# Optimization experiments

Measured on AMD Instinct MI355X. Metric: run time of the kernel, lower is better.

Reference implementation:

```python
import jax, jax.numpy as jnp
import numpy as np

H, D, K = 8, 64, 9           # new num heads, head size, conv kernel size
A = H * D                    # all_head_size = 512
HID = 2 * A                  # input hidden size = 1024
STD = 0.02


def setup_inputs() -> dict:
    key = jax.random.key(0)
    ks = jax.random.split(key, 16)
    B, S = 4, 2048
    f = jnp.float32
    inp = {
        'hidden_states': jax.random.normal(ks[0], (B, S, HID), f),
        'Wq': jax.random.normal(ks[1], (A, A), f) * STD,
        'bq': jnp.zeros((A,), f),
        'Wk': jax.random.normal(ks[2], (A, A), f) * STD,
        'bk': jnp.zeros((A,), f),
        'Wv': jax.random.normal(ks[3], (A, A), f) * STD,
        'bv': jnp.zeros((A,), f),
        'dw_w': jax.random.normal(ks[4], (A, 1, K), f) * STD,   # depthwise conv (groups=A)
        'pw_w': jax.random.normal(ks[5], (A, A, 1), f) * STD,   # pointwise 1x1 conv
        'sep_b': jnp.zeros((A, 1), f),                          # SeparableConv1D bias
        'Wck': jax.random.normal(ks[6], (H * K, A), f) * STD,   # conv_kernel_layer
        'bck': jnp.zeros((H * K,), f),
        'Wco': jax.random.normal(ks[7], (A, A), f) * STD,       # conv_out_layer
        'bco': jnp.zeros((A,), f),
    }
    return inp


def reference(hidden_states, Wq, bq, Wk, bk, Wv, bv, dw_w, pw_w, sep_b, Wck, bck, Wco, bco):
    B, S, _ = hidden_states.shape
    hs_attn = hidden_states[:, :, :A]
    hs_conv = hidden_states[:, :, A:]

    q = hs_attn @ Wq.T + bq
    k = hs_attn @ Wk.T + bk
    v = hs_attn @ Wv.T + bv

    # SeparableConv1D on (B, A, S): depthwise then pointwise, plus bias
    x = hs_conv.transpose(0, 2, 1)
    x = jax.lax.conv_general_dilated(
        x, dw_w, window_strides=(1,), padding=[(K // 2, K // 2)],
        feature_group_count=A, dimension_numbers=('NCH', 'OIH', 'NCH'))
    x = jnp.einsum('bcs,oc->bos', x, pw_w[:, :, 0]) + sep_b
    mixed_key_conv = x.transpose(0, 2, 1)            # (B,S,A)

    # per-token softmax conv kernel
    conv_attn = mixed_key_conv * hs_conv
    ckl = (conv_attn @ Wck.T + bck).reshape(B, S, H, K)
    ckl = jax.nn.softmax(ckl, axis=-1)               # softmax over kernel taps

    # dynamic-span lightweight convolution (unfold -> batched matmul)
    col = hs_conv @ Wco.T + bco                      # (B,S,A)
    pad = jnp.pad(col, ((0, 0), (K // 2, K // 2), (0, 0)))
    windows = jnp.stack([pad[:, i:i + S] for i in range(K)], axis=-1)  # (B,S,A,K)
    windows = windows.reshape(B, S, H, D, K)
    conv_out = jnp.einsum('bshdk,bshk->bshd', windows, ckl)            # (B,S,H,D)

    # standard self-attention
    qh = q.reshape(B, S, H, D).transpose(0, 2, 1, 3)
    kh = k.reshape(B, S, H, D).transpose(0, 2, 1, 3)
    vh = v.reshape(B, S, H, D).transpose(0, 2, 1, 3)
    scale = jnp.asarray(1.0 / np.sqrt(D), q.dtype)
    scores = jnp.einsum('bhqd,bhkd->bhqk', qh, kh) * scale
    probs = jax.nn.softmax(scores, axis=-1)
    ctx = jnp.einsum('bhqk,bhkd->bqhd', probs, vh)   # (B,S,H,D)

    out = jnp.concatenate([ctx, conv_out], axis=2)   # (B,S,2H,D)
    return out.reshape(B, S, HID)
```

## Files before the change

kernel.cpp:

```cpp
#include <hip/hip_runtime.h>
#include <hip/hip_bf16.h>

#define NH   8
#define HD   64
#define KW   9
#define AD   512
#define HIDD 1024
#define BB   4
#define SS   2048
#define MTOK (BB*SS)
#define WSZ  262144

typedef __attribute__((ext_vector_type(8))) short short8;
typedef __attribute__((ext_vector_type(4))) float floatx4;
typedef __attribute__((ext_vector_type(16))) float floatx16;

__device__ __forceinline__ short f2bf(float f) {
    unsigned u = __float_as_uint(f);
    u = (u + 0x7FFFu + ((u >> 16) & 1u)) >> 16;
    return (short)u;
}
__device__ __forceinline__ float bf2f(short s) {
    return __uint_as_float(((unsigned)(unsigned short)s) << 16);
}
__device__ __forceinline__ float exp2_raw(float x) {
    return __builtin_amdgcn_exp2f(x);
}
__device__ __forceinline__ unsigned pkbf2(float a, float b) {
    unsigned d;
    asm("v_cvt_pk_bf16_f32 %0, %1, %2" : "=v"(d) : "v"(a), "v"(b));
    return d;
}
__device__ __forceinline__ void gl2lds16(const short* g, short* l) {
    __builtin_amdgcn_global_load_lds(
        (const __attribute__((address_space(1))) void*)g,
        (__attribute__((address_space(3))) void*)l, 16, 0, 0);
}

__global__ __launch_bounds__(256) void prep_kernel(
    const float* __restrict__ hs,
    const float* __restrict__ pw, const float* __restrict__ Wco,
    const float* __restrict__ Wq, const float* __restrict__ Wk,
    const float* __restrict__ Wv, const float* __restrict__ Wck,
    const float* __restrict__ dw,
    short* __restrict__ hsb, short* __restrict__ wb, short* __restrict__ x1)
{
    __shared__ float wl[KW * AD];
    const int bid = blockIdx.x, tid = threadIdx.x;

    if (bid < 4096) {
        int idx = bid * 256 + tid;
        const float* s = hs + (long)idx * 8;
        float4 a = *(const float4*)s, c = *(const float4*)(s + 4);
        short8 o;
        o[0]=f2bf(a.x); o[1]=f2bf(a.y); o[2]=f2bf(a.z); o[3]=f2bf(a.w);
        o[4]=f2bf(c.x); o[5]=f2bf(c.y); o[6]=f2bf(c.z); o[7]=f2bf(c.w);
        *(short8*)(hsb + (long)idx * 8) = o;
    } else if (bid < 4768) {
        int idx = (bid - 4096) * 256 + tid;
        int e0 = idx * 8;
        short8 o;
        if (e0 < 5 * WSZ) {
            int w = e0 >> 18, off = e0 & (WSZ - 1);
            const float* src = (w == 0) ? pw : (w == 1) ? Wco : (w == 2) ? Wq
                             : (w == 3) ? Wk : Wv;
            float4 a = *(const float4*)(src + off), c = *(const float4*)(src + off + 4);
            o[0]=f2bf(a.x); o[1]=f2bf(a.y); o[2]=f2bf(a.z); o[3]=f2bf(a.w);
            o[4]=f2bf(c.x); o[5]=f2bf(c.y); o[6]=f2bf(c.z); o[7]=f2bf(c.w);
        } else {
            int off = e0 - 5 * WSZ;
            int row = off >> 9, col = off & 511;
            if (row < NH * KW) {
                const float* src = Wck + row * AD + col;
                float4 a = *(const float4*)src, c = *(const float4*)(src + 4);
                o[0]=f2bf(a.x); o[1]=f2bf(a.y); o[2]=f2bf(a.z); o[3]=f2bf(a.w);
                o[4]=f2bf(c.x); o[5]=f2bf(c.y); o[6]=f2bf(c.z); o[7]=f2bf(c.w);
            } else {
                for (int i = 0; i < 8; ++i) o[i] = 0;
            }
        }
        *(short8*)(wb + e0) = o;
    } else {
        for (int t = tid; t < KW * AD; t += 256) {
            int c = t / KW, k = t - c * KW;
            wl[k * AD + c] = dw[t];
        }
        __syncthreads();
        int idx = (bid - 4768) * 256 + tid;
        int c8  = (idx & 63) * 8;
        int tok = idx >> 6;
        int s   = tok & (SS - 1);
        int b   = tok >> 11;
        const float* base = hs + (long)(b * SS) * HIDD + AD + c8;
        float acc[8];
#pragma unroll
        for (int i = 0; i < 8; ++i) acc[i] = 0.f;
#pragma unroll
        for (int kk = 0; kk < KW; ++kk) {
            int ss2 = s + kk - KW / 2;
            if (ss2 >= 0 && ss2 < SS) {
                const float* hp = base + (long)ss2 * HIDD;
                float4 h0 = *(const float4*)hp;
                float4 h1 = *(const float4*)(hp + 4);
                float4 w0 = *(const float4*)(wl + kk * AD + c8);
                float4 w1 = *(const float4*)(wl + kk * AD + c8 + 4);
                acc[0] += w0.x * h0.x; acc[1] += w0.y * h0.y;
                acc[2] += w0.z * h0.z; acc[3] += w0.w * h0.w;
                acc[4] += w1.x * h1.x; acc[5] += w1.y * h1.y;
                acc[6] += w1.z * h1.z; acc[7] += w1.w * h1.w;
            }
        }
        short8 o;
#pragma unroll
        for (int i = 0; i < 8; ++i) o[i] = f2bf(acc[i]);
        *(short8*)(x1 + (long)tok * AD + c8) = o;
    }
}

template<int FM, int FN, int MODE>
__device__ __forceinline__ void gemm_body(
    int bx, int by, short* Sm,
    const short* __restrict__ X, int ldx, int xoff,
    const short* __restrict__ W,
    const float* __restrict__ b0p, const float* __restrict__ b1p,
    const float* __restrict__ b2p,
    const short* __restrict__ mulp, int mul_ld, int mul_off,
    void* __restrict__ Cout, short* __restrict__ vtout,
    int ldc, int N, int Kd, float oscale)
{
    constexpr int TM = 32 * FM, TN = 32 * FN;
    constexpr int SLOT = (TM + TN) * 64;
    const int tid  = threadIdx.x;
    const int wv   = tid >> 6, lane = tid & 63;
    const int ln   = lane & 15, quad = lane >> 4;
    const int wm   = wv >> 1, wn = wv & 1;
    const int m0 = bx * TM, n0 = by * TN;

    floatx4 acc[FM][FN];
#pragma unroll
    for (int i = 0; i < FM; ++i)
#pragma unroll
        for (int j = 0; j < FN; ++j) acc[i][j] = (floatx4){0.f, 0.f, 0.f, 0.f};

    const short* xbase = X + (long)m0 * ldx + xoff;
    const short* wbase = W + (long)n0 * Kd;

    auto stage = [&](int k0, int slot) {
        short* As = Sm + slot * SLOT;
        short* Bs = As + TM * 64;
#pragma unroll
        for (int g = tid; g < TM * 8; g += 256) {
            int m = g >> 3, p = g & 7, gk = p ^ (m & 7);
            gl2lds16(xbase + (long)m * ldx + k0 + gk * 8, &As[g * 8]);
        }
#pragma unroll
        for (int g = tid; g < TN * 8; g += 256) {
            int m = g >> 3, p = g & 7, gk = p ^ (m & 7);
            gl2lds16(wbase + (long)m * Kd + k0 + gk * 8, &Bs[g * 8]);
        }
    };
    auto compute = [&](int slot) {
        const short* As = Sm + slot * SLOT;
        const short* Bs = As + TM * 64;
#pragma unroll
        for (int half = 0; half < 2; ++half) {
            short8 afr[FM], bfr[FN];
#pragma unroll
            for (int i = 0; i < FM; ++i) {
                int p = (half * 4 + quad) ^ (ln & 7);
                afr[i] = *(const short8*)&As[(wm * 16 * FM + i * 16 + ln) * 64 + p * 8];
            }
#pragma unroll
            for (int j = 0; j < FN; ++j) {
                int p = (half * 4 + quad) ^ (ln & 7);
                bfr[j] = *(const short8*)&Bs[(wn * 16 * FN + j * 16 + ln) * 64 + p * 8];
            }
#pragma unroll
            for (int i = 0; i < FM; ++i)
#pragma unroll
                for (int j = 0; j < FN; ++j)
                    acc[i][j] = __builtin_amdgcn_mfma_f32_16x16x32_bf16(
                        afr[i], bfr[j], acc[i][j], 0, 0, 0);
        }
    };

    stage(0, 0);
    asm volatile("s_waitcnt vmcnt(0)" ::: "memory");
    __builtin_amdgcn_s_barrier();
    asm volatile("" ::: "memory");

    const int nk = Kd >> 6;
    int slot = 0;
    for (int t = 0; t < nk - 1; ++t) {
        stage((t + 1) * 64, slot ^ 1);
        compute(slot);
        asm volatile("s_waitcnt vmcnt(0)" ::: "memory");
        __builtin_amdgcn_s_barrier();
        asm volatile("" ::: "memory");
        slot ^= 1;
    }
    compute(slot);

    if constexpr (MODE == 3) {
        if (n0 >= 1024) {
            __syncthreads();
            short* T = Sm;
#pragma unroll
            for (int j = 0; j < FN; ++j) {
                int nl = wn * 16 * FN + j * 16 + ln;
                float bv = b2p[n0 - 1024 + nl];
#pragma unroll
                for (int i = 0; i < FM; ++i) {
                    int ml = wm * 16 * FM + i * 16 + quad * 4;
                    unsigned lo = pkbf2(acc[i][j][0] + bv, acc[i][j][1] + bv);
                    unsigned hi = pkbf2(acc[i][j][2] + bv, acc[i][j][3] + bv);
                    *(unsigned*)&T[nl * 130 + ml]     = lo;
                    *(unsigned*)&T[nl * 130 + ml + 2] = hi;
                }
            }
            __syncthreads();
            int nl = tid >> 1, hf = tid & 1;
            int nn = n0 - 1024 + nl;
            int hh2 = nn >> 6, dd = nn & 63;
            int bidx = m0 >> 11, sblk = m0 & (SS - 1);
            short* dst = vtout + ((long)((bidx * NH + hh2) * HD + dd)) * SS
                       + sblk + hf * 64;
            const short* src = &T[nl * 130 + hf * 64];
#pragma unroll
            for (int u = 0; u < 8; ++u) {
                uint4 v;
                v.x = *(const unsigned*)&src[u * 8 + 0];
                v.y = *(const unsigned*)&src[u * 8 + 2];
                v.z = *(const unsigned*)&src[u * 8 + 4];
                v.w = *(const unsigned*)&src[u * 8 + 6];
                *(uint4*)(dst + u * 8) = v;
            }
            return;
        }
#pragma unroll
        for (int j = 0; j < FN; ++j) {
            int n = n0 + wn * 16 * FN + j * 16 + ln;
            float bv = (n < 512) ? b0p[n] : b1p[n - 512];
            float sc = (n < 512) ? oscale : 1.f;
#pragma unroll
            for (int i = 0; i < FM; ++i) {
#pragma unroll
                for (int r = 0; r < 4; ++r) {
                    int m = m0 + wm * 16 * FM + i * 16 + quad * 4 + r;
                    float val = (acc[i][j][r] + bv) * sc;
                    ((short*)Cout)[(long)m * ldc + n] = f2bf(val);
                }
            }
        }
        return;
    }

#pragma unroll
    for (int j = 0; j < FN; ++j) {
        int n = n0 + wn * 16 * FN + j * 16 + ln;
        if (n < N) {
            float bv = b0p[n], sc = oscale;
#pragma unroll
            for (int i = 0; i < FM; ++i) {
#pragma unroll
                for (int r = 0; r < 4; ++r) {
                    int m = m0 + wm * 16 * FM + i * 16 + quad * 4 + r;
                    float val = (acc[i][j][r] + bv) * sc;
                    if constexpr (MODE == 2)
                        val *= bf2f(mulp[(long)m * mul_ld + mul_off + n]);
                    if constexpr (MODE == 0)
                        ((float*)Cout)[(long)m * ldc + n] = val;
                    else
                        ((short*)Cout)[(long)m * ldc + n] = f2bf(val);
                }
            }
        }
    }
}

__global__ __launch_bounds__(256) void mega1_kernel(
    const short* __restrict__ hsb, const short* __restrict__ x1c,
    const short* __restrict__ Wqkv_b, const short* __restrict__ pw_b,
    const float* __restrict__ bq, const float* __restrict__ bk,
    const float* __restrict__ bv, const float* __restrict__ sepb,
    short* __restrict__ qkvb, short* __restrict__ vTb,
    short* __restrict__ cabO, float oscale)
{
    __shared__ __align__(16) char smem[65536];
    int bid = blockIdx.x;
    if (bid < 768) {
        gemm_body<4, 4, 3>(bid & 63, bid >> 6, (short*)smem,
            hsb, HIDD, 0, Wqkv_b, bq, bk, bv, nullptr, 0, 0,
            qkvb, vTb, 1536, 1536, AD, oscale);
    } else {
        int id = bid - 768;
        gemm_body<4, 2, 2>(id & 63, id >> 6, (short*)smem,
            x1c, AD, 0, pw_b, sepb, nullptr, nullptr, hsb, HIDD, AD,
            cabO, nullptr, 2048, AD, AD, 1.f);
    }
}

__global__ __launch_bounds__(256) void mega3_kernel(
    const short* __restrict__ qkv, const short* __restrict__ vT,
    const short* __restrict__ hsb, const short* __restrict__ cabO,
    const short* __restrict__ Wco_b, const short* __restrict__ Wck_b,
    const float* __restrict__ bco, const float* __restrict__ bck,
    short* __restrict__ x1c, float* __restrict__ cklp,
    float* __restrict__ out)
{
    __shared__ __align__(16) char smem[49664];
    const int bid = blockIdx.x;
    const int tid = threadIdx.x;

    if (bid >= 512) {
        if (bid < 1024) {
            int id = bid - 512;
            gemm_body<4, 2, 1>(id & 63, id >> 6, (short*)smem,
                hsb, HIDD, AD, Wco_b, bco, nullptr, nullptr, nullptr, 0, 0,
                x1c, nullptr, AD, AD, AD, 1.f);
        } else {
            int id = bid - 1024;
            gemm_body<2, 2, 0>(id & 127, id >> 7, (short*)smem,
                cabO, 2048, 0, Wck_b, bck, nullptr, nullptr, nullptr, 0, 0,
                cklp, nullptr, NH * KW, NH * KW, AD, 1.f);
        }
        return;
    }

    short* const KbB = (short*)smem;
    short* const VbB = (short*)smem + 3 * 4096;
    float* const ls  = (float*)(smem + 49152);

    const int qt = bid & 15, h = (bid >> 4) & 7, b = bid >> 7;
    const int w    = tid >> 6;
    const int lane = tid & 63;
    const int l5   = lane & 31;
    const int hh   = lane >> 5;

    const int  q0 = qt * 128 + w * 32;
    const long rowbase = (long)b * SS;

    short8 qf[4];
    {
        const short* qrow = qkv + (rowbase + q0 + l5) * 1536 + h * HD;
#pragma unroll
        for (int i = 0; i < 4; ++i)
            qf[i] = *(const short8*)(qrow + i * 16 + hh * 8);
    }

    floatx16 acc0, acc1;
    floatx16 Z;
#pragma unroll
    for (int r = 0; r < 16; ++r) { acc0[r] = 0.f; acc1[r] = 0.f; Z[r] = 0.f; }
    float l_i = 0.f;

    const int m1 = tid >> 3,  gk1 = (tid & 7) ^ (m1 & 7);
    const int g2 = 256 + tid;
    const int m2 = g2 >> 3,   gk2 = (g2 & 7) ^ (m2 & 7);
    const short* kbase  = qkv + 512 + rowbase * 1536 + h * HD;
    const short* vtbase = vT + ((long)(b * NH + h) * HD) * SS;
    const short* sk0 = kbase  + (long)m1 * 1536 + gk1 * 8;
    const short* sk1 = kbase  + (long)m2 * 1536 + gk2 * 8;
    const short* sv0 = vtbase + (long)m1 * SS   + gk1 * 8;
    const short* sv1 = vtbase + (long)m2 * SS   + gk2 * 8;

    auto STAGE_K = [&](int slot, bool adv) {
        gl2lds16(sk0, KbB + slot * 4096 + tid * 8);
        gl2lds16(sk1, KbB + slot * 4096 + g2 * 8);
        if (adv) { sk0 += 64 * 1536; sk1 += 64 * 1536; }
    };
    auto STAGE_V = [&](int slot) {
        gl2lds16(sv0, VbB + slot * 4096 + tid * 8);
        gl2lds16(sv1, VbB + slot * 4096 + g2 * 8);
        sv0 += 64; sv1 += 64;
    };

    auto qkt = [&](const short* KB, floatx16& S0, floatx16& S1) {
        {
            int p = hh ^ (l5 & 7);
            short8 k0 = *(const short8*)&KB[l5 * 64 + p * 8];
            short8 k1 = *(const short8*)&KB[(32 + l5) * 64 + p * 8];
            S0 = __builtin_amdgcn_mfma_f32_32x32x16_bf16(k0, qf[0], Z, 0, 0, 0);
            S1 = __builtin_amdgcn_mfma_f32_32x32x16_bf16(k1, qf[0], Z, 0, 0, 0);
        }
#pragma unroll
        for (int i = 1; i < 4; ++i) {
            int p = (2 * i + hh) ^ (l5 & 7);
            short8 k0 = *(const short8*)&KB[l5 * 64 + p * 8];
            short8 k1 = *(const short8*)&KB[(32 + l5) * 64 + p * 8];
            S0 = __builtin_amdgcn_mfma_f32_32x32x16_bf16(k0, qf[i], S0, 0, 0, 0);
            S1 = __builtin_amdgcn_mfma_f32_32x32x16_bf16(k1, qf[i], S1, 0, 0, 0);
        }
    };

    auto smax = [&](const floatx16& S0, const floatx16& S1, short8* pf) {
        float pe0[16], pe1[16];
#pragma unroll
        for (int r = 0; r < 16; ++r) {
            pe0[r] = exp2_raw(S0[r]);
            pe1[r] = exp2_raw(S1[r]);
        }
        float s = 0.f;
#pragma unroll
        for (int r = 0; r < 16; ++r) s += pe0[r] + pe1[r];
        l_i += s;
#pragma unroll
        for (int t = 0; t < 2; ++t) {
            const float* pe = t ? pe1 : pe0;
#pragma unroll
            for (int u = 0; u < 2; ++u) {
                unsigned a0 = pkbf2(pe[8 * u + 0], pe[8 * u + 1]);
                unsigned a1 = pkbf2(pe[8 * u + 2], pe[8 * u + 3]);
                unsigned b0 = pkbf2(pe[8 * u + 4], pe[8 * u + 5]);
                unsigned b1 = pkbf2(pe[8 * u + 6], pe[8 * u + 7]);
                asm("v_permlane32_swap_b32 %0, %1" : "+v"(a0), "+v"(b0));
                asm("v_permlane32_swap_b32 %0, %1" : "+v"(a1), "+v"(b1));
                union { uint4 u4; short8 s8; } cv;
                cv.u4 = make_uint4(a0, a1, b0, b1);
                pf[t * 2 + u] = cv.s8;
            }
        }
    };

    auto pv = [&](const short* VB, const short8* pf) {
#pragma unroll
        for (int s = 0; s < 4; ++s) {
            int p = (2 * s + hh) ^ (l5 & 7);
            short8 v0 = *(const short8*)&VB[l5 * 64 + p * 8];
            short8 v1 = *(const short8*)&VB[(32 + l5) * 64 + p * 8];
            acc0 = __builtin_amdgcn_mfma_f32_32x32x16_bf16(pf[s], v0, acc0, 0, 0, 0);
            acc1 = __builtin_amdgcn_mfma_f32_32x32x16_bf16(pf[s], v1, acc1, 0, 0, 0);
        }
    };

    short8 pfA[4], pfB[4];

    STAGE_K(0, true);
    STAGE_K(1, true);
    STAGE_V(0);
    asm volatile("s_waitcnt vmcnt(0)" ::: "memory");
    __builtin_amdgcn_s_barrier();
    asm volatile("" ::: "memory");

    {
        STAGE_K(2, true);
        STAGE_V(1);
        floatx16 S0, S1;
        qkt(KbB, S0, S1);
        smax(S0, S1, pfA);
        asm volatile("s_waitcnt vmcnt(4)" ::: "memory");
        __builtin_amdgcn_s_barrier();
        asm volatile("" ::: "memory");
    }

#define PHASE(KS, VPS, KST, VST, KADV, PIN, POUT)                      \
    {                                                                  \
        STAGE_K(KST, KADV);                                            \
        STAGE_V(VST);                                                  \
        floatx16 S0, S1;                                               \
        __builtin_amdgcn_s_setprio(1);                                 \
        qkt(KbB + (KS) * 4096, S0, S1);                                \
        pv(VbB + (VPS) * 4096, PIN);                                   \
        __builtin_amdgcn_s_setprio(0);                                 \
        smax(S0, S1, POUT);                                            \
        asm volatile("s_waitcnt vmcnt(4)" ::: "memory");               \
        __builtin_amdgcn_s_barrier();                                  \
        asm volatile("" ::: "memory");                                 \
    }

    for (int g = 0; g < 5; ++g) {
        bool notlast = (g < 4);
        PHASE(1, 0, 0, 2, true,    pfA, pfB);
        PHASE(2, 1, 1, 0, true,    pfB, pfA);
        PHASE(0, 2, 2, 1, true,    pfA, pfB);
        PHASE(1, 0, 0, 2, true,    pfB, pfA);
        PHASE(2, 1, 1, 0, notlast, pfA, pfB);
        PHASE(0, 2, 2, 1, notlast, pfB, pfA);
    }
#undef PHASE

    {
        floatx16 S0, S1;
        __builtin_amdgcn_s_setprio(1);
        qkt(KbB + 1 * 4096, S0, S1);
        pv(VbB + 0 * 4096, pfA);
        __builtin_amdgcn_s_setprio(0);
        smax(S0, S1, pfB);
        asm volatile("s_waitcnt vmcnt(0)" ::: "memory");
        __builtin_amdgcn_s_barrier();
        asm volatile("" ::: "memory");
    }
    pv(VbB + 1 * 4096, pfB);

    l_i += __shfl_xor(l_i, 32);
    ls[w * 32 + l5] = 1.f / l_i;
    float4 lv[4];
#pragma unroll
    for (int g = 0; g < 4; ++g)
        lv[g] = *(const float4*)&ls[w * 32 + 8 * g + 4 * hh];

#pragma unroll
    for (int r = 0; r < 16; ++r) {
        int g = r >> 2, j = r & 3;
        int qr = j + 8 * g + 4 * hh;
        float iv = lv[g][j];
        float* orow = out + (rowbase + q0 + qr) * HIDD + h * HD;
        orow[l5]      = acc0[r] * iv;
        orow[32 + l5] = acc1[r] * iv;
    }
}

__global__ __launch_bounds__(256) void convout_kernel(
    const short* __restrict__ col, const float* __restrict__ ckl,
    float* __restrict__ out)
{
    int idx = blockIdx.x * 256 + threadIdx.x;
    int d8  = (idx & 63) * 8;
    int tok = idx >> 6;
    int s   = tok & (SS - 1);
    int b   = tok >> 11;
    int h   = d8 >> 6;
    const float* lg = ckl + (long)tok * (NH * KW) + h * KW;
    float wv[KW];
    float mx = -1e30f;
#pragma unroll
    for (int i = 0; i < KW; ++i) { wv[i] = lg[i]; mx = fmaxf(mx, wv[i]); }
    float sum = 0.f;
#pragma unroll
    for (int i = 0; i < KW; ++i) { wv[i] = __expf(wv[i] - mx); sum += wv[i]; }
    float inv = 1.f / sum;
    float a[8];
#pragma unroll
    for (int i = 0; i < 8; ++i) a[i] = 0.f;
    const short* cbase = col + (long)(b * SS) * AD + d8;
#pragma unroll
    for (int kk = 0; kk < KW; ++kk) {
        int ss2 = s + kk - KW / 2;
        if (ss2 >= 0 && ss2 < SS) {
            uint4 cv = *(const uint4*)(cbase + (long)ss2 * AD);
            float w = wv[kk];
            a[0] += w * bf2f((short)(cv.x & 0xFFFF));
            a[1] += w * bf2f((short)(cv.x >> 16));
            a[2] += w * bf2f((short)(cv.y & 0xFFFF));
            a[3] += w * bf2f((short)(cv.y >> 16));
            a[4] += w * bf2f((short)(cv.z & 0xFFFF));
            a[5] += w * bf2f((short)(cv.z >> 16));
            a[6] += w * bf2f((short)(cv.w & 0xFFFF));
            a[7] += w * bf2f((short)(cv.w >> 16));
        }
    }
    float* op = &out[(long)tok * HIDD + AD + d8];
    *(float4*)op       = make_float4(a[0]*inv, a[1]*inv, a[2]*inv, a[3]*inv);
    *(float4*)(op + 4) = make_float4(a[4]*inv, a[5]*inv, a[6]*inv, a[7]*inv);
}

extern "C" void kernel_launch(void* const* d_in, const int* in_sizes, int n_in,
                              void* d_out, int out_size, void* d_ws, size_t ws_size,
                              hipStream_t stream)
{
    const float* hs   = (const float*)d_in[0];
    const float* Wq   = (const float*)d_in[1];
    const float* bq   = (const float*)d_in[2];
    const float* Wk   = (const float*)d_in[3];
    const float* bk   = (const float*)d_in[4];
    const float* Wv   = (const float*)d_in[5];
    const float* bv   = (const float*)d_in[6];
    const float* dw   = (const float*)d_in[7];
    const float* pw   = (const float*)d_in[8];
    const float* sepb = (const float*)d_in[9];
    const float* Wck  = (const float*)d_in[10];
    const float* bck  = (const float*)d_in[11];
    const float* Wco  = (const float*)d_in[12];
    const float* bco  = (const float*)d_in[13];
    float* out = (float*)d_out;

    short* hsb  = (short*)d_ws;
    short* x1c  = hsb + (long)MTOK * HIDD;
    short* qkvb = x1c + (long)MTOK * AD;
    short* vTb  = qkvb + (long)MTOK * 1536;
    float* ckl  = (float*)(vTb + (long)MTOK * AD);
    short* wb   = (short*)(ckl + (long)MTOK * (NH * KW));
    short* pw_b   = wb;
    short* Wco_b  = wb + 1L * WSZ;
    short* Wqkv_b = wb + 2L * WSZ;
    short* Wck_b  = wb + 5L * WSZ;
    short* cabO   = (short*)d_out + 1024;

    const float QSCALE = 0.18033688011112042f;

    prep_kernel<<<6816, 256, 0, stream>>>(
        hs, pw, Wco, Wq, Wk, Wv, Wck, dw, hsb, wb, x1c);
    mega1_kernel<<<1280, 256, 0, stream>>>(
        hsb, x1c, Wqkv_b, pw_b, bq, bk, bv, sepb, qkvb, vTb, cabO, QSCALE);
    mega3_kernel<<<1280, 256, 0, stream>>>(
        qkvb, vTb, hsb, cabO, Wco_b, Wck_b, bco, bck, x1c, ckl, out);
    convout_kernel<<<MTOK * AD / 2048, 256, 0, stream>>>(x1c, ckl, out);

    (void)in_sizes; (void)n_in; (void)out_size; (void)ws_size;
}
```

Baseline: 200.8 us.

## Fuse conv-half bf16 cast into depthwise conv and add triple-buffered GEMM

```diff
diff --git a/kernel.cpp b/kernel.cpp
--- a/kernel.cpp
+++ b/kernel.cpp
@@ -48,16 +48,18 @@
     __shared__ float wl[KW * AD];
     const int bid = blockIdx.x, tid = threadIdx.x;
 
-    if (bid < 4096) {
+    if (bid < 2048) {
         int idx = bid * 256 + tid;
-        const float* s = hs + (long)idx * 8;
+        int c8  = (idx & 63) * 8;
+        int tok = idx >> 6;
+        const float* s = hs + (long)tok * HIDD + c8;
         float4 a = *(const float4*)s, c = *(const float4*)(s + 4);
         short8 o;
         o[0]=f2bf(a.x); o[1]=f2bf(a.y); o[2]=f2bf(a.z); o[3]=f2bf(a.w);
         o[4]=f2bf(c.x); o[5]=f2bf(c.y); o[6]=f2bf(c.z); o[7]=f2bf(c.w);
-        *(short8*)(hsb + (long)idx * 8) = o;
-    } else if (bid < 4768) {
-        int idx = (bid - 4096) * 256 + tid;
+        *(short8*)(hsb + (long)tok * HIDD + c8) = o;
+    } else if (bid < 2720) {
+        int idx = (bid - 2048) * 256 + tid;
         int e0 = idx * 8;
         short8 o;
         if (e0 < 5 * WSZ) {
@@ -86,13 +88,14 @@
             wl[k * AD + c] = dw[t];
         }
         __syncthreads();
-        int idx = (bid - 4768) * 256 + tid;
+        int idx = (bid - 2720) * 256 + tid;
         int c8  = (idx & 63) * 8;
         int tok = idx >> 6;
         int s   = tok & (SS - 1);
         int b   = tok >> 11;
         const float* base = hs + (long)(b * SS) * HIDD + AD + c8;
         float acc[8];
+        float4 ch0, ch1;
 #pragma unroll
         for (int i = 0; i < 8; ++i) acc[i] = 0.f;
 #pragma unroll
@@ -102,6 +105,7 @@
                 const float* hp = base + (long)ss2 * HIDD;
                 float4 h0 = *(const float4*)hp;
                 float4 h1 = *(const float4*)(hp + 4);
+                if (kk == KW / 2) { ch0 = h0; ch1 = h1; }
                 float4 w0 = *(const float4*)(wl + kk * AD + c8);
                 float4 w1 = *(const float4*)(wl + kk * AD + c8 + 4);
                 acc[0] += w0.x * h0.x; acc[1] += w0.y * h0.y;
@@ -114,6 +118,10 @@
 #pragma unroll
         for (int i = 0; i < 8; ++i) o[i] = f2bf(acc[i]);
         *(short8*)(x1 + (long)tok * AD + c8) = o;
+        short8 oc;
+        oc[0]=f2bf(ch0.x); oc[1]=f2bf(ch0.y); oc[2]=f2bf(ch0.z); oc[3]=f2bf(ch0.w);
+        oc[4]=f2bf(ch1.x); oc[5]=f2bf(ch1.y); oc[6]=f2bf(ch1.z); oc[7]=f2bf(ch1.w);
+        *(short8*)(hsb + (long)tok * HIDD + AD + c8) = oc;
     }
 }
 
@@ -278,6 +286,125 @@
     }
 }
 
+template<int FM, int FN, int MODE>
+__device__ __forceinline__ void gemm_ring(
+    int bx, int by, short* Sm,
+    const short* __restrict__ X, int ldx, int xoff,
+    const short* __restrict__ W,
+    const float* __restrict__ b0p,
+    const short* __restrict__ mulp, int mul_ld, int mul_off,
+    void* __restrict__ Cout, int ldc, int N, int Kd, float oscale)
+{
+    constexpr int TM = 32 * FM, TN = 32 * FN;
+    constexpr int SLOT = (TM + TN) * 64;
+    constexpr int LPT  = (TM + TN) * 8 / 256;
+    const int tid  = threadIdx.x;
+    const int wv   = tid >> 6, lane = tid & 63;
+    const int ln   = lane & 15, quad = lane >> 4;
+    const int wm   = wv >> 1, wn = wv & 1;
+    const int m0 = bx * TM, n0 = by * TN;
+
+    floatx4 acc[FM][FN];
+#pragma unroll
+    for (int i = 0; i < FM; ++i)
+#pragma unroll
+        for (int j = 0; j < FN; ++j) acc[i][j] = (floatx4){0.f, 0.f, 0.f, 0.f};
+
+    const short* xbase = X + (long)m0 * ldx + xoff;
+    const short* wbase = W + (long)n0 * Kd;
+
+    auto stage = [&](int k0, int slot) {
+        short* As = Sm + slot * SLOT;
+        short* Bs = As + TM * 64;
+#pragma unroll
+        for (int g = tid; g < TM * 8; g += 256) {
+            int m = g >> 3, p = g & 7, gk = p ^ (m & 7);
+            gl2lds16(xbase + (long)m * ldx + k0 + gk * 8, &As[g * 8]);
+        }
+#pragma unroll
+        for (int g = tid; g < TN * 8; g += 256) {
+            int m = g >> 3, p = g & 7, gk = p ^ (m & 7);
+            gl2lds16(wbase + (long)m * Kd + k0 + gk * 8, &Bs[g * 8]);
+        }
+    };
+    auto compute = [&](int slot) {
+        const short* As = Sm + slot * SLOT;
+        const short* Bs = As + TM * 64;
+#pragma unroll
+        for (int half = 0; half < 2; ++half) {
+            short8 afr[FM], bfr[FN];
+#pragma unroll
+            for (int i = 0; i < FM; ++i) {
+                int p = (half * 4 + quad) ^ (ln & 7);
+                afr[i] = *(const short8*)&As[(wm * 16 * FM + i * 16 + ln) * 64 + p * 8];
+            }
+#pragma unroll
+            for (int j = 0; j < FN; ++j) {
+                int p = (half * 4 + quad) ^ (ln & 7);
+                bfr[j] = *(const short8*)&Bs[(wn * 16 * FN + j * 16 + ln) * 64 + p * 8];
+            }
+#pragma unroll
+            for (int i = 0; i < FM; ++i)
+#pragma unroll
+                for (int j = 0; j < FN; ++j)
+                    acc[i][j] = __builtin_amdgcn_mfma_f32_16x16x32_bf16(
+                        afr[i], bfr[j], acc[i][j], 0, 0, 0);
+        }
+    };
+    auto wait_lpt = [&]() {
+        if constexpr (LPT == 6)
+            asm volatile("s_waitcnt vmcnt(6)" ::: "memory");
+        else if constexpr (LPT == 4)
+            asm volatile("s_waitcnt vmcnt(4)" ::: "memory");
+        else
+            asm volatile("s_waitcnt vmcnt(0)" ::: "memory");
+    };
+
+    const int nk = Kd >> 6;
+    stage(0, 0);
+    stage(64, 1);
+    wait_lpt();
+    __builtin_amdgcn_s_barrier();
+    asm volatile("" ::: "memory");
+
+    for (int t = 0; t < nk; ++t) {
+        bool more = (t + 2 < nk);
+        if (more) stage((t + 2) * 64, (t + 2) % 3);
+        compute(t % 3);
+        if (more) {
+            wait_lpt();
+            __builtin_amdgcn_s_barrier();
+            asm volatile("" ::: "memory");
+        } else if (t + 1 < nk) {
+            asm volatile("s_waitcnt vmcnt(0)" ::: "memory");
+            __builtin_amdgcn_s_barrier();
+            asm volatile("" ::: "memory");
+        }
+    }
+
+#pragma unroll
+    for (int j = 0; j < FN; ++j) {
+        int n = n0 + wn * 16 * FN + j * 16 + ln;
+        if (n < N) {
+            float bv = b0p[n];
+#pragma unroll
+            for (int i = 0; i < FM; ++i) {
+#pragma unroll
+                for (int r = 0; r < 4; ++r) {
+                    int m = m0 + wm * 16 * FM + i * 16 + quad * 4 + r;
+                    float val = (acc[i][j][r] + bv) * oscale;
+                    if constexpr (MODE == 2)
+                        val *= bf2f(mulp[(long)m * mul_ld + mul_off + n]);
+                    if constexpr (MODE == 0)
+                        ((float*)Cout)[(long)m * ldc + n] = val;
+                    else
+                        ((short*)Cout)[(long)m * ldc + n] = f2bf(val);
+                }
+            }
+        }
+    }
+}
+
 __global__ __launch_bounds__(256) void mega1_kernel(
     const short* __restrict__ hsb, const short* __restrict__ x1c,
     const short* __restrict__ Wqkv_b, const short* __restrict__ pw_b,
@@ -286,7 +413,7 @@
     short* __restrict__ qkvb, short* __restrict__ vTb,
     short* __restrict__ cabO, float oscale)
 {
-    __shared__ __align__(16) char smem[65536];
+    __shared__ __align__(16) char smem[73728];
     int bid = blockIdx.x;
     if (bid < 768) {
         gemm_body<4, 4, 3>(bid & 63, bid >> 6, (short*)smem,
@@ -294,9 +421,9 @@
             qkvb, vTb, 1536, 1536, AD, oscale);
     } else {
         int id = bid - 768;
-        gemm_body<4, 2, 2>(id & 63, id >> 6, (short*)smem,
-            x1c, AD, 0, pw_b, sepb, nullptr, nullptr, hsb, HIDD, AD,
-            cabO, nullptr, 2048, AD, AD, 1.f);
+        gemm_ring<4, 2, 2>(id & 63, id >> 6, (short*)smem,
+            x1c, AD, 0, pw_b, sepb, hsb, HIDD, AD,
+            cabO, 2048, AD, AD, 1.f);
     }
 }
 
@@ -320,9 +447,9 @@
                 x1c, nullptr, AD, AD, AD, 1.f);
         } else {
             int id = bid - 1024;
-            gemm_body<2, 2, 0>(id & 127, id >> 7, (short*)smem,
-                cabO, 2048, 0, Wck_b, bck, nullptr, nullptr, nullptr, 0, 0,
-                cklp, nullptr, NH * KW, NH * KW, AD, 1.f);
+            gemm_ring<2, 2, 0>(id & 127, id >> 7, (short*)smem,
+                cabO, 2048, 0, Wck_b, bck, nullptr, 0, 0,
+                cklp, NH * KW, NH * KW, AD, 1.f);
         }
         return;
     }
@@ -588,7 +715,7 @@
 
     const float QSCALE = 0.18033688011112042f;
 
-    prep_kernel<<<6816, 256, 0, stream>>>(
+    prep_kernel<<<4768, 256, 0, stream>>>(
         hs, pw, Wco, Wq, Wk, Wv, Wck, dw, hsb, wb, x1c);
     mega1_kernel<<<1280, 256, 0, stream>>>(
         hsb, x1c, Wqkv_b, pw_b, bq, bk, bv, sepb, qkvb, vTb, cabO, QSCALE);
```

Result: no change. 202.4 us (+0.8%).
